# Performance work log

Hardware: AMD Instinct MI355X
Metric: run time of the kernel (lower is better)

Reference implementation:

```python
import jax, jax.numpy as jnp
import numpy as np

PI = 3.141592653589793
TAU = 0.5          # gumbel-softmax temperature
EPS = 1e-6
B, N, D = 128, 32, 256

def _linear(x, w, b=None):
    y = x @ w.T
    return y if b is None else y + b

def _wrap(a):
    return (a + PI) % (2 * PI) - PI

def setup_inputs() -> dict:
    key = jax.random.key(0)
    ks = jax.random.split(key, 16)
    s = 0.05
    return {
        "embedding": jax.random.normal(ks[0], (B, N, 11), jnp.float32),
        "gumbel_u": jax.random.uniform(ks[1], (B * N, N - 1, 2), jnp.float32),
        "emb1_w": jax.random.normal(ks[2], (128, 5), jnp.float32) * s,
        "emb1_b": jnp.zeros((128,), jnp.float32),
        "emb2_w": jax.random.normal(ks[3], (D, 128), jnp.float32) * s,
        "emb2_b": jnp.zeros((D,), jnp.float32),
        "hm1_w": jax.random.normal(ks[4], (D, D + 7), jnp.float32) * s,
        "hm1_b": jnp.zeros((D,), jnp.float32),
        "hm2_w": jax.random.normal(ks[5], (D, D), jnp.float32) * s,
        "hm2_b": jnp.zeros((D,), jnp.float32),
        "he_w": jax.random.normal(ks[6], (2, D), jnp.float32) * s,
        "he_b": jnp.zeros((2,), jnp.float32),
        "q_w": jax.random.normal(ks[7], (D, D), jnp.float32) * s,
        "k_w": jax.random.normal(ks[8], (D, 10), jnp.float32) * s,
        "v_w": jax.random.normal(ks[9], (D, 10), jnp.float32) * s,
        "v_b": jnp.zeros((D,), jnp.float32),
        "dec_w": jax.random.normal(ks[10], (2 * D, 2 * D), jnp.float32) * s,
        "dec_b": jnp.zeros((2 * D,), jnp.float32),
    }

def reference(embedding, gumbel_u, emb1_w, emb1_b, emb2_w, emb2_b,
              hm1_w, hm1_b, hm2_w, hm2_b, he_w, he_b,
              q_w, k_w, v_w, v_b, dec_w, dec_b):
    b, n, _ = embedding.shape
    d = q_w.shape[0]
    # static off-diagonal index lists (i,j), j != i, row-major like mask indexing
    rows, cols = np.nonzero(~np.eye(n, dtype=bool))

    embed = embedding[:, :, 4:9].reshape(b * n, 5)
    position = embedding[:, :, :2]
    heading = embedding[:, :, 2:4]
    action = embedding[:, :, 7:9]
    goal = embedding[:, :, -2:]

    # agent embedding MLP (leaky_relu slope 0.01, torch default)
    h = jax.nn.leaky_relu(_linear(embed, emb1_w, emb1_b))
    agent_embed = jax.nn.leaky_relu(_linear(h, emb2_w, emb2_b)).reshape(b, n, d)

    # pairwise geometry  [b,i,j,...]
    rel_vec = position[:, None, :, :] - position[:, :, None, :]   # pos_j - pos_i
    dx, dy = rel_vec[..., 0], rel_vec[..., 1]
    rel_dist = jnp.linalg.norm(rel_vec, axis=-1, keepdims=True) / 12.0
    heading_angle_i = jnp.arctan2(heading[..., 1], heading[..., 0])[:, :, None]  # [b,n,1]
    angle = _wrap(jnp.arctan2(dy, dx) - heading_angle_i)
    hj_cos = jnp.broadcast_to(heading[:, None, :, 0], (b, n, n))
    hj_sin = jnp.broadcast_to(heading[:, None, :, 1], (b, n, n))
    action_j = jnp.broadcast_to(action[:, None, :, :], (b, n, n, 2))
    edge_features = jnp.concatenate([
        rel_dist, jnp.cos(angle)[..., None], jnp.sin(angle)[..., None],
        hj_cos[..., None], hj_sin[..., None], action_j], axis=-1)  # [b,n,n,7]

    # hard attention branch (off-diagonal pairs only)
    h_i_flat = jnp.broadcast_to(agent_embed[:, :, None, :], (b, n, n - 1, d)).reshape(b * n, n - 1, d)
    edge_flat = edge_features[:, rows, cols].reshape(b * n, n - 1, 7)
    hard_input = jnp.concatenate([h_i_flat, edge_flat], axis=-1)
    h_hard = _linear(jax.nn.relu(_linear(hard_input, hm1_w, hm1_b)), hm2_w, hm2_b)
    hard_logits = _linear(h_hard, he_w, he_b)                      # [b*n, n-1, 2]
    g = -jnp.log(-jnp.log(gumbel_u + 1e-10) + 1e-10)
    hard_soft = jax.nn.softmax((hard_logits + g) / TAU, axis=-1)
    hard_weights = hard_soft[..., 1].reshape(b, n, n - 1)

    unnorm = jnp.linalg.norm(rel_vec, axis=-1, keepdims=True)      # [b,n,n,1]
    unnorm_rel_dist = unnorm[:, rows, cols].reshape(b * n, n - 1, 1)

    # goal polar features
    goal_rel_vec = goal[:, None, :, :] - position[:, :, None, :]   # [b,n,n,2]
    goal_rel_dist = jnp.linalg.norm(goal_rel_vec, axis=-1, keepdims=True)
    goal_rel_angle = _wrap(jnp.arctan2(goal_rel_vec[..., 1], goal_rel_vec[..., 0]) - heading_angle_i)
    goal_polar = jnp.concatenate([goal_rel_dist, jnp.cos(goal_rel_angle)[..., None],
                                  jnp.sin(goal_rel_angle)[..., None]], axis=-1)
    soft_edge = jnp.concatenate([edge_features, goal_polar], axis=-1)  # [b,n,n,10]

    # soft attention (vectorized over agents; off-diagonal gather)
    q = agent_embed @ q_w.T                                         # [b,n,d]
    k = soft_edge @ k_w.T                                           # [b,n,n,d]
    v = jax.nn.relu(_linear(soft_edge, v_w, v_b))                   # [b,n,n,d]
    k_off = k[:, rows, cols].reshape(b, n, n - 1, d)
    v_off = v[:, rows, cols].reshape(b, n, n - 1, d)
    score = jnp.einsum('bnd,bnjd->bnj', q, k_off) / jnp.sqrt(jnp.float32(d))
    soft_w = jax.nn.softmax(score, axis=-1)
    combined = soft_w * hard_weights                                # [b,n,n-1]
    x = jnp.einsum('bnjd,bnj->bnd', v_off, combined).reshape(b * n, d)

    final_input = jnp.concatenate([agent_embed.reshape(b * n, d), x], axis=-1)
    output = _linear(final_input, dec_w, dec_b)                     # [b*n, 2d]

    cwn = combined / (combined.sum(axis=-1, keepdims=True) + EPS)
    mean_entropy = (-(cwn * jnp.log(cwn + EPS)).sum(axis=-1)).mean()
    comb_w = combined.reshape(n, -1)  # matches torch.stack(dim=1).reshape(n, -1)

    return (output, hard_logits[..., 1], unnorm_rel_dist, mean_entropy, hard_weights, comb_w)
```

## Files before the change

### kernel.cpp

```cpp
#include <hip/hip_runtime.h>
#include <hip/hip_bf16.h>
#include <math.h>

typedef __hip_bfloat16 bf16;
typedef short bf16x8 __attribute__((ext_vector_type(8)));
typedef float f32x4 __attribute__((ext_vector_type(4)));
typedef unsigned short u16;

#define R_TOT 4096
#define NJ 31

#define OFF_AE   0
#define OFF_QK   1048576
#define OFF_S1   2097152
#define OFF_ENT  4542464
#define OFF_X    4546560
#define OFF_W    5595136
#define W_E1W   0
#define W_E1B   640
#define W_E2P   768
#define W_E2B   33536
#define W_H1B   101120
#define W_W1EP  167684
#define W_HE2P  171780
#define W_CB    173828
#define W_S1P   200452
#define W_VW    235780
#define W_VB    238340
#define W_DECWT 238596
#define W_DECB  500740
#define W_QKM   501252

#define OUT0 0
#define OUT1 2097152
#define OUT2 2224128
#define OUT3 2351104
#define OUT4 2351105
#define OUT5 2478081

__device__ __forceinline__ float b2f(bf16 x) { return __bfloat162float(x); }
__device__ __forceinline__ float ldin(const void* p, int i, int flag) {
    return flag ? b2f(((const bf16*)p)[i]) : ((const float*)p)[i];
}
__device__ __forceinline__ void stout(void* p, int i, float v, int flag) {
    if (flag) ((bf16*)p)[i] = __float2bfloat16(v);
    else      ((float*)p)[i] = v;
}
__device__ __forceinline__ u16 f2bbits(float v) {
    bf16 h = __float2bfloat16(v);
    return *(u16*)&h;
}
__device__ __forceinline__ int detect_flag(const void* emb) {
    float x = ((const float*)emb)[threadIdx.x & 63];
    int sane = (x == x) && (fabsf(x) < 1e20f);
    unsigned long long m = __ballot(sane);
    return (__popcll(m) == 64) ? 0 : 1;
}

__global__ __launch_bounds__(256) void k_prep(
        const void* emb,
        const void* e1w, const void* e1b, const void* e2w, const void* e2b,
        const void* h1w, const void* h1b, const void* h2w, const void* h2b,
        const void* hew, const void* heb, const void* qw,  const void* kw,
        const void* vw,  const void* vb,  const void* decw,const void* decb,
        float* W) {
    int flag = detect_flag(emb);
    int blk = blockIdx.x;
    int tid = threadIdx.x;
    if (blk < 2048) {
        int idx = blk * 256 + tid;
        if (idx < 262144) {
            int jj   = idx & 7;
            int lane = (idx >> 3) & 63;
            int tile = idx >> 9;
            int nt = tile & 31, kt = tile >> 5;
            int n = nt * 16 + (lane & 15);
            int k = kt * 32 + ((lane >> 4) << 3) + jj;
            ((u16*)(W + W_DECWT))[idx] = f2bbits(ldin(decw, n * 512 + k, flag));
        }
        int j = idx - 262144;
        if (j >= 0 && j < 98304) {
            int p;
            const void* src; int ldm, Wdst;
            if (j < 32768)      { p = j;          src = e2w; ldm = 128; Wdst = W_E2P; }
            else                { p = j - 32768;  src = h1w; ldm = 263; Wdst = W_S1P; }
            int jj   = p & 7;
            int lane = (p >> 3) & 63;
            int tile = p >> 9;
            int nt = tile & 15, kt = tile >> 4;
            int n = nt * 16 + (lane & 15);
            int k = kt * 32 + ((lane >> 4) << 3) + jj;
            ((u16*)(W + Wdst))[p] = f2bbits(ldin(src, n * ldm + k, flag));
        } else if (j >= 98304 && j < 102912) {
            int q2 = j - 98304;
            if      (q2 < 640)   W[W_E1W  + q2]           = ldin(e1w,  q2,          flag);
            else if (q2 < 768)   W[W_E1B  + (q2 - 640)]   = ldin(e1b,  q2 - 640,    flag);
            else if (q2 < 1024)  W[W_E2B  + (q2 - 768)]   = ldin(e2b,  q2 - 768,    flag);
            else if (q2 < 1280)  W[W_H1B  + (q2 - 1024)]  = ldin(h1b,  q2 - 1024,   flag);
            else if (q2 < 3840)  W[W_VW   + (q2 - 1280)]  = ldin(vw,   q2 - 1280,   flag);
            else if (q2 < 4096)  W[W_VB   + (q2 - 3840)]  = ldin(vb,   q2 - 3840,   flag);
            else                 W[W_DECB + (q2 - 4096)]  = ldin(decb, q2 - 4096,   flag);
        }
    } else if (blk < 2304) {
        int p = (blk - 2048) * 16 + (tid >> 4);
        int l = tid & 15;
        int jj = p & 7, lane = (p >> 3) & 63, kt = p >> 9;
        int k = kt * 32 + ((lane >> 4) << 3) + jj;
        int n = lane & 15;
        float v = 0.f;
        if (n < 10) {
#pragma unroll
            for (int dd = 0; dd < 16; dd++) {
                int d = l + 16 * dd;
                v += ldin(qw, d * 256 + k, flag) * ldin(kw, d * 10 + n, flag);
            }
        }
        v += __shfl_xor(v, 1, 64); v += __shfl_xor(v, 2, 64);
        v += __shfl_xor(v, 4, 64); v += __shfl_xor(v, 8, 64);
        if (l == 0) ((u16*)(W + W_QKM))[p] = f2bbits(v);
    } else if (blk < 2560) {
        int q = (blk - 2304) * 16 + (tid >> 4);
        int l = tid & 15;
        int jj = q & 7, lane = (q >> 3) & 63, kt = q >> 9;
        int n = lane & 15;
        int c = kt * 32 + ((lane >> 4) << 3) + jj;
        float v = 0.f;
        if (n < 2) {
#pragma unroll
            for (int dd = 0; dd < 16; dd++) {
                int d = l + 16 * dd;
                v += ldin(hew, n * 256 + d, flag) * ldin(h2w, d * 256 + c, flag);
            }
        }
        v += __shfl_xor(v, 1, 64); v += __shfl_xor(v, 2, 64);
        v += __shfl_xor(v, 4, 64); v += __shfl_xor(v, 8, 64);
        if (l == 0) ((u16*)(W + W_HE2P))[q] = f2bbits(v);
    } else if (blk < 2592) {
        int p = (blk - 2560) * 256 + tid;
        int jj = p & 7, lane = (p >> 3) & 63, nt = p >> 9;
        int n = nt * 16 + (lane & 15);
        int k = ((lane >> 4) << 3) + jj;
        float v = (k < 7) ? ldin(h1w, n * 263 + 256 + k, flag) : 0.f;
        ((u16*)(W + W_W1EP))[p] = f2bbits(v);
    } else {
        if (tid < 32) {
            int i = tid >> 4, l = tid & 15;
            float v = 0.f;
#pragma unroll
            for (int dd = 0; dd < 16; dd++) {
                int d = l + 16 * dd;
                v += ldin(hew, i * 256 + d, flag) * ldin(h2b, d, flag);
            }
            v += __shfl_xor(v, 1, 64); v += __shfl_xor(v, 2, 64);
            v += __shfl_xor(v, 4, 64); v += __shfl_xor(v, 8, 64);
            if (l == 0) W[W_CB + i] = v + ldin(heb, i, flag);
        }
    }
}

__global__ __launch_bounds__(256) void k_embed(const void* emb, const float* W,
                                               u16* aeb, float* qkws, float* s1ws) {
    int flag = detect_flag(emb);
    int r0 = blockIdx.x * 16;
    __shared__ float embL[16][12];
    __shared__ u16 hB[16][136];
    __shared__ u16 aeB[16][264];
    int tid = threadIdx.x;
    for (int idx = tid; idx < 16 * 11; idx += 256) {
        int s = idx / 11, t = idx % 11;
        embL[s][t] = ldin(emb, (r0 + s) * 11 + t, flag);
    }
    __syncthreads();
    for (int idx = tid; idx < 16 * 128; idx += 256) {
        int s = idx >> 7, jo = idx & 127;
        float v = W[W_E1B + jo];
#pragma unroll
        for (int t = 0; t < 5; t++) v += W[W_E1W + jo * 5 + t] * embL[s][4 + t];
        hB[s][jo] = f2bbits(v > 0.f ? v : 0.01f * v);
    }
    __syncthreads();
    int wv = tid >> 6, ln = tid & 63;
    int lr = ln & 15, quad = ln >> 4;
    {
        const bf16x8* Bp = (const bf16x8*)(W + W_E2P);
        f32x4 acc[4];
#pragma unroll
        for (int nt = 0; nt < 4; nt++) acc[nt] = (f32x4){0.f, 0.f, 0.f, 0.f};
#pragma unroll
        for (int kt = 0; kt < 4; kt++) {
            bf16x8 af = *(const bf16x8*)&hB[lr][kt * 32 + (quad << 3)];
#pragma unroll
            for (int nt = 0; nt < 4; nt++) {
                bf16x8 bfr = Bp[(kt * 16 + (wv * 4 + nt)) * 64 + ln];
                acc[nt] = __builtin_amdgcn_mfma_f32_16x16x32_bf16(af, bfr, acc[nt], 0, 0, 0);
            }
        }
#pragma unroll
        for (int nt = 0; nt < 4; nt++) {
            int d = wv * 64 + nt * 16 + lr;
            float bias = W[W_E2B + d];
#pragma unroll
            for (int reg = 0; reg < 4; reg++) {
                int m = quad * 4 + reg;
                float v = acc[nt][reg] + bias;
                v = v > 0.f ? v : 0.01f * v;
                u16 bits = f2bbits(v);
                aeB[m][d] = bits;
                aeb[(r0 + m) * 256 + d] = bits;
            }
        }
    }
    __syncthreads();
    {
        const bf16x8* Bs = (const bf16x8*)(W + W_S1P);
        f32x4 sac[4];
#pragma unroll
        for (int nt = 0; nt < 4; nt++) sac[nt] = (f32x4){0.f, 0.f, 0.f, 0.f};
#pragma unroll
        for (int kt = 0; kt < 8; kt++) {
            bf16x8 af = *(const bf16x8*)&aeB[lr][kt * 32 + (quad << 3)];
#pragma unroll
            for (int nt = 0; nt < 4; nt++) {
                bf16x8 bs = Bs[(kt * 16 + (wv * 4 + nt)) * 64 + ln];
                sac[nt] = __builtin_amdgcn_mfma_f32_16x16x32_bf16(af, bs, sac[nt], 0, 0, 0);
            }
        }
#pragma unroll
        for (int nt = 0; nt < 4; nt++) {
            int d = wv * 64 + nt * 16 + lr;
            float bias = W[W_H1B + d];
#pragma unroll
            for (int reg = 0; reg < 4; reg++) {
                int m = quad * 4 + reg;
                s1ws[(r0 + m) * 256 + d] = sac[nt][reg] + bias;
            }
        }
        if (wv == 0) {
            const bf16x8* Bm = (const bf16x8*)(W + W_QKM);
            f32x4 qk = (f32x4){0.f, 0.f, 0.f, 0.f};
#pragma unroll
            for (int kt = 0; kt < 8; kt++) {
                bf16x8 af = *(const bf16x8*)&aeB[lr][kt * 32 + (quad << 3)];
                qk = __builtin_amdgcn_mfma_f32_16x16x32_bf16(af, Bm[kt * 64 + ln], qk, 0, 0, 0);
            }
            if (lr < 10) {
#pragma unroll
                for (int reg = 0; reg < 4; reg++) {
                    int m = quad * 4 + reg;
                    qkws[(r0 + m) * 10 + lr] = qk[reg];
                }
            }
        }
    }
}

__global__ __launch_bounds__(256) void k_fused(const void* emb, const void* gum,
                                               const float* s1ws, const float* qkws, const float* W,
                                               u16* xb, float* entws, void* out) {
    int flag = detect_flag(emb);
    int r = blockIdx.x;
    int b = r >> 5, i = r & 31;
    __shared__ float embB[32][12];
    __shared__ float seL[32][10];
    __shared__ u16 eA[32][32];
    __shared__ u16 a1[32][264];
    __shared__ float pj[4][32][2];
    __shared__ float cL[32];
    __shared__ float qkL[10];
    int tid = threadIdx.x;
    for (int idx = tid; idx < 32 * 11; idx += 256) {
        int s = idx / 11, t = idx % 11;
        embB[s][t] = ldin(emb, (b * 32 + s) * 11 + t, flag);
    }
    for (int idx = tid; idx < 32 * 32; idx += 256) ((u16*)eA)[idx] = 0;
    if (tid >= 64 && tid < 74) qkL[tid - 64] = qkws[r * 10 + (tid - 64)];
    __syncthreads();
    if (tid < NJ) {
        int jp = tid;
        int j = jp + (jp >= i ? 1 : 0);
        float pix = embB[i][0], piy = embB[i][1], hix = embB[i][2], hiy = embB[i][3];
        float pjx = embB[j][0], pjy = embB[j][1], hjx = embB[j][2], hjy = embB[j][3];
        float ajx = embB[j][7], ajy = embB[j][8];
        float gjx = embB[j][9], gjy = embB[j][10];
        float dx = pjx - pix, dy = pjy - piy;
        float dist = sqrtf(dx * dx + dy * dy);
        float hai = atan2f(hiy, hix);
        float ang = atan2f(dy, dx) - hai;
        float gx = gjx - pix, gy = gjy - piy;
        float gdist = sqrtf(gx * gx + gy * gy);
        float gang = atan2f(gy, gx) - hai;
        float f[10];
        f[0] = dist * (1.f / 12.f);
        f[1] = cosf(ang); f[2] = sinf(ang);
        f[3] = hjx; f[4] = hjy; f[5] = ajx; f[6] = ajy;
        f[7] = gdist; f[8] = cosf(gang); f[9] = sinf(gang);
#pragma unroll
        for (int t = 0; t < 10; t++) seL[jp][t] = f[t];
#pragma unroll
        for (int t = 0; t < 7; t++) eA[jp][t] = f2bbits(f[t]);
        stout(out, OUT2 + r * NJ + jp, dist, flag);
    }
    __syncthreads();
    int wv = tid >> 6, ln = tid & 63;
    int lr = ln & 15, quad = ln >> 4;
    {
        const bf16x8* Bp = (const bf16x8*)(W + W_W1EP);
        bf16x8 af0 = *(const bf16x8*)&eA[lr][quad << 3];
        bf16x8 af1 = *(const bf16x8*)&eA[16 + lr][quad << 3];
#pragma unroll
        for (int nt = 0; nt < 4; nt++) {
            int gnt = wv * 4 + nt;
            int d = gnt * 16 + lr;
            float s1v = s1ws[r * 256 + d];
            f32x4 acc0 = (f32x4){s1v, s1v, s1v, s1v};
            f32x4 acc1 = acc0;
            bf16x8 bb = Bp[gnt * 64 + ln];
            acc0 = __builtin_amdgcn_mfma_f32_16x16x32_bf16(af0, bb, acc0, 0, 0, 0);
            acc1 = __builtin_amdgcn_mfma_f32_16x16x32_bf16(af1, bb, acc1, 0, 0, 0);
#pragma unroll
            for (int reg = 0; reg < 4; reg++) {
                a1[(quad << 2) + reg][d]      = f2bbits(fmaxf(acc0[reg], 0.f));
                a1[16 + (quad << 2) + reg][d] = f2bbits(fmaxf(acc1[reg], 0.f));
            }
        }
    }
    __syncthreads();
    {
        const bf16x8* Ep = (const bf16x8*)(W + W_HE2P);
        f32x4 l0 = (f32x4){0.f, 0.f, 0.f, 0.f};
        f32x4 l1 = (f32x4){0.f, 0.f, 0.f, 0.f};
#pragma unroll
        for (int kk = 0; kk < 2; kk++) {
            int kt = wv * 2 + kk;
            bf16x8 a0 = *(const bf16x8*)&a1[lr][kt * 32 + (quad << 3)];
            bf16x8 a1f = *(const bf16x8*)&a1[16 + lr][kt * 32 + (quad << 3)];
            bf16x8 bb = Ep[kt * 64 + ln];
            l0 = __builtin_amdgcn_mfma_f32_16x16x32_bf16(a0, bb, l0, 0, 0, 0);
            l1 = __builtin_amdgcn_mfma_f32_16x16x32_bf16(a1f, bb, l1, 0, 0, 0);
        }
        if (lr < 2) {
#pragma unroll
            for (int reg = 0; reg < 4; reg++) {
                pj[wv][(quad << 2) + reg][lr]      = l0[reg];
                pj[wv][16 + (quad << 2) + reg][lr] = l1[reg];
            }
        }
    }
    __syncthreads();
    if (wv == 0) {
        float hwv = 0.f;
        if (ln < NJ) {
            float p0 = pj[0][ln][0] + pj[1][ln][0] + pj[2][ln][0] + pj[3][ln][0];
            float p1 = pj[0][ln][1] + pj[1][ln][1] + pj[2][ln][1] + pj[3][ln][1];
            float l0 = p0 + W[W_CB + 0], l1 = p1 + W[W_CB + 1];
            float u0 = ldin(gum, (r * NJ + ln) * 2 + 0, flag);
            float u1 = ldin(gum, (r * NJ + ln) * 2 + 1, flag);
            float g0 = -logf(-logf(u0 + 1e-10f) + 1e-10f);
            float g1 = -logf(-logf(u1 + 1e-10f) + 1e-10f);
            float dl = ((l1 + g1) - (l0 + g0)) * 2.0f;
            hwv = 1.f / (1.f + expf(-dl));
            stout(out, OUT1 + r * NJ + ln, l1, flag);
            stout(out, OUT4 + r * NJ + ln, hwv, flag);
        }
        float sc = -1e30f;
        if (ln < NJ) {
            float p = 0.f;
#pragma unroll
            for (int t = 0; t < 10; t++) p += qkL[t] * seL[ln][t];
            sc = p * (1.f / 16.f);
        }
        float m = sc;
#pragma unroll
        for (int s = 32; s >= 1; s >>= 1) m = fmaxf(m, __shfl_xor(m, s, 64));
        float e = (ln < NJ) ? expf(sc - m) : 0.f;
        float sum = e;
#pragma unroll
        for (int s = 32; s >= 1; s >>= 1) sum += __shfl_xor(sum, s, 64);
        float sw = e / sum;
        float cmb = sw * hwv;
        if (ln < NJ) {
            cL[ln] = cmb;
            stout(out, OUT5 + r * NJ + ln, cmb, flag);
        }
        float csum = cmb;
#pragma unroll
        for (int s = 32; s >= 1; s >>= 1) csum += __shfl_xor(csum, s, 64);
        float cwn = cmb / (csum + 1e-6f);
        float et = (ln < NJ) ? -cwn * logf(cwn + 1e-6f) : 0.f;
#pragma unroll
        for (int s = 32; s >= 1; s >>= 1) et += __shfl_xor(et, s, 64);
        if (ln == 0) entws[r] = et;
    }
    __syncthreads();
    float vwr[10];
#pragma unroll
    for (int t = 0; t < 10; t++) vwr[t] = W[W_VW + tid * 10 + t];
    float vbv = W[W_VB + tid];
    float x = 0.f;
    for (int j = 0; j < NJ; j++) {
        float v = vbv;
#pragma unroll
        for (int t = 0; t < 10; t++) v += vwr[t] * seL[j][t];
        v = fmaxf(v, 0.f);
        x += v * cL[j];
    }
    xb[r * 256 + tid] = f2bbits(x);
}

__global__ __launch_bounds__(256) void k_dec(const void* emb, const u16* aeb, const u16* xb,
                                             const float* W, const float* entws, void* out) {
    int flag = detect_flag(emb);
    int r0 = (blockIdx.x >> 2) * 32;
    int nq = blockIdx.x & 3;
    __shared__ u16 finB[32][520];
    int tid = threadIdx.x;
    for (int idx = tid; idx < 32 * 512; idx += 256) {
        int s = idx >> 9, c = idx & 511;
        finB[s][c] = (c < 256) ? aeb[(r0 + s) * 256 + c] : xb[(r0 + s) * 256 + (c - 256)];
    }
    __syncthreads();
    int wv = tid >> 6, ln = tid & 63;
    int lr = ln & 15, quad = ln >> 4;
    const bf16x8* Bp = (const bf16x8*)(W + W_DECWT);
    f32x4 acc[2][2];
#pragma unroll
    for (int mt = 0; mt < 2; mt++)
#pragma unroll
        for (int nt = 0; nt < 2; nt++) acc[mt][nt] = (f32x4){0.f, 0.f, 0.f, 0.f};
#pragma unroll
    for (int kt = 0; kt < 16; kt++) {
        bf16x8 af[2];
#pragma unroll
        for (int mt = 0; mt < 2; mt++)
            af[mt] = *(const bf16x8*)&finB[mt * 16 + lr][kt * 32 + (quad << 3)];
#pragma unroll
        for (int nt = 0; nt < 2; nt++) {
            int gnt = nq * 8 + wv * 2 + nt;
            bf16x8 bfr = Bp[(kt * 32 + gnt) * 64 + ln];
#pragma unroll
            for (int mt = 0; mt < 2; mt++)
                acc[mt][nt] = __builtin_amdgcn_mfma_f32_16x16x32_bf16(af[mt], bfr, acc[mt][nt], 0, 0, 0);
        }
    }
#pragma unroll
    for (int nt = 0; nt < 2; nt++) {
        int d = (nq * 8 + wv * 2 + nt) * 16 + lr;
        float bias = W[W_DECB + d];
#pragma unroll
        for (int mt = 0; mt < 2; mt++)
#pragma unroll
            for (int reg = 0; reg < 4; reg++) {
                int m = mt * 16 + quad * 4 + reg;
                stout(out, OUT0 + (r0 + m) * 512 + d, acc[mt][nt][reg] + bias, flag);
            }
    }
    if (blockIdx.x == 0) {
        __shared__ float red[4];
        float s = 0.f;
        for (int i2 = tid; i2 < R_TOT; i2 += 256) s += entws[i2];
#pragma unroll
        for (int m = 32; m >= 1; m >>= 1) s += __shfl_xor(s, m, 64);
        if ((tid & 63) == 0) red[tid >> 6] = s;
        __syncthreads();
        if (tid == 0) {
            float t = red[0] + red[1] + red[2] + red[3];
            stout(out, OUT3, t / (float)R_TOT, flag);
        }
    }
}

extern "C" void kernel_launch(void* const* d_in, const int* in_sizes, int n_in,
                              void* d_out, int out_size, void* d_ws, size_t ws_size,
                              hipStream_t stream) {
    const void* emb  = d_in[0];
    const void* gum  = d_in[1];
    const void* e1w  = d_in[2];
    const void* e1b  = d_in[3];
    const void* e2w  = d_in[4];
    const void* e2b  = d_in[5];
    const void* h1w  = d_in[6];
    const void* h1b  = d_in[7];
    const void* h2w  = d_in[8];
    const void* h2b  = d_in[9];
    const void* hew  = d_in[10];
    const void* heb  = d_in[11];
    const void* qw   = d_in[12];
    const void* kw   = d_in[13];
    const void* vw   = d_in[14];
    const void* vb   = d_in[15];
    const void* decw = d_in[16];
    const void* decb = d_in[17];

    float* wsf = (float*)d_ws;
    u16*   aeb  = (u16*)(wsf + OFF_AE);
    float* qkws = wsf + OFF_QK;
    float* s1ws = wsf + OFF_S1;
    float* entw = wsf + OFF_ENT;
    u16*   xb   = (u16*)(wsf + OFF_X);
    float* W    = wsf + OFF_W;

    hipLaunchKernelGGL(k_prep, dim3(2593), dim3(256), 0, stream,
                       emb, e1w, e1b, e2w, e2b, h1w, h1b, h2w, h2b, hew, heb,
                       qw, kw, vw, vb, decw, decb, W);
    hipLaunchKernelGGL(k_embed, dim3(256), dim3(256), 0, stream, emb, W, aeb, qkws, s1ws);
    hipLaunchKernelGGL(k_fused, dim3(4096), dim3(256), 0, stream,
                       emb, gum, s1ws, qkws, W, xb, entw, d_out);
    hipLaunchKernelGGL(k_dec, dim3(512), dim3(256), 0, stream, emb, aeb, xb, W, entw, d_out);
}
```

Before: 161.1 us.

## Merge four kernels into one persistent kernel with software grid barriers

Replaces the four separate launches (weight prep, embed, fused attention, decoder) with a single persistent kernel of 512 blocks. The stages are separated by an atomic-counter grid barrier, and blocks loop over the former grid sizes. This removes launch gaps and per-kernel tail effects between stages. In exchange it adds barrier spin costs and a memset launch, caps parallelism at 512 blocks for the 4096-block fused stage, and relies on every block being co-resident, which risks deadlock if they are not.

```diff
diff --git a/kernel.cpp b/kernel.cpp
--- a/kernel.cpp
+++ b/kernel.cpp
@@ -9,6 +9,7 @@
 
 #define R_TOT 4096
 #define NJ 31
+#define GRID_N 512
 
 #define OFF_AE   0
 #define OFF_QK   1048576
@@ -30,6 +31,7 @@
 #define W_DECWT 238596
 #define W_DECB  500740
 #define W_QKM   501252
+#define OFF_BAR  6100992
 
 #define OUT0 0
 #define OUT1 2097152
@@ -57,414 +59,425 @@
     return (__popcll(m) == 64) ? 0 : 1;
 }
 
-__global__ __launch_bounds__(256) void k_prep(
-        const void* emb,
+__device__ __forceinline__ void grid_sync(int* bar) {
+    __syncthreads();
+    if (threadIdx.x == 0) {
+        __threadfence();
+        int gen = __hip_atomic_load(bar + 1, __ATOMIC_RELAXED, __HIP_MEMORY_SCOPE_AGENT);
+        int arrived = __hip_atomic_fetch_add(bar, 1, __ATOMIC_ACQ_REL, __HIP_MEMORY_SCOPE_AGENT);
+        if (arrived == GRID_N - 1) {
+            __hip_atomic_store(bar, 0, __ATOMIC_RELAXED, __HIP_MEMORY_SCOPE_AGENT);
+            __hip_atomic_fetch_add(bar + 1, 1, __ATOMIC_RELEASE, __HIP_MEMORY_SCOPE_AGENT);
+        } else {
+            while (__hip_atomic_load(bar + 1, __ATOMIC_ACQUIRE, __HIP_MEMORY_SCOPE_AGENT) == gen)
+                __builtin_amdgcn_s_sleep(2);
+        }
+        __threadfence();
+    }
+    __syncthreads();
+}
+
+struct EmbedS { float embL[16][12]; u16 hB[16][136]; u16 aeB[16][264]; };
+struct FusedS { float embB[32][12]; float seL[32][10]; u16 eA[32][32];
+                u16 a1[32][264]; float pj[4][32][2]; float cL[32]; float qkL[10]; };
+struct DecS   { u16 finB[32][520]; float red[4]; };
+union SharedU { EmbedS e; FusedS f; DecS d; };
+
+__global__ __launch_bounds__(256, 2) void k_mega(
+        const void* emb, const void* gum,
         const void* e1w, const void* e1b, const void* e2w, const void* e2b,
         const void* h1w, const void* h1b, const void* h2w, const void* h2b,
         const void* hew, const void* heb, const void* qw,  const void* kw,
         const void* vw,  const void* vb,  const void* decw,const void* decb,
-        float* W) {
+        float* W, u16* aeb, float* qkws, float* s1ws, float* entws, u16* xb,
+        int* bar, void* out) {
+    __shared__ SharedU sh;
     int flag = detect_flag(emb);
-    int blk = blockIdx.x;
     int tid = threadIdx.x;
-    if (blk < 2048) {
-        int idx = blk * 256 + tid;
-        if (idx < 262144) {
-            int jj   = idx & 7;
-            int lane = (idx >> 3) & 63;
-            int tile = idx >> 9;
-            int nt = tile & 31, kt = tile >> 5;
-            int n = nt * 16 + (lane & 15);
+    int wv = tid >> 6, ln = tid & 63;
+    int lr = ln & 15, quad = ln >> 4;
+
+    for (int blk = blockIdx.x; blk < 2593; blk += GRID_N) {
+        if (blk < 2048) {
+            int idx = blk * 256 + tid;
+            if (idx < 262144) {
+                int jj   = idx & 7;
+                int lane = (idx >> 3) & 63;
+                int tile = idx >> 9;
+                int nt = tile & 31, kt = tile >> 5;
+                int n = nt * 16 + (lane & 15);
+                int k = kt * 32 + ((lane >> 4) << 3) + jj;
+                ((u16*)(W + W_DECWT))[idx] = f2bbits(ldin(decw, n * 512 + k, flag));
+            }
+            int j = idx - 262144;
+            if (j >= 0 && j < 98304) {
+                int p;
+                const void* src; int ldm, Wdst;
+                if (j < 32768)      { p = j;          src = e2w; ldm = 128; Wdst = W_E2P; }
+                else                { p = j - 32768;  src = h1w; ldm = 263; Wdst = W_S1P; }
+                int jj   = p & 7;
+                int lane = (p >> 3) & 63;
+                int tile = p >> 9;
+                int nt = tile & 15, kt = tile >> 4;
+                int n = nt * 16 + (lane & 15);
+                int k = kt * 32 + ((lane >> 4) << 3) + jj;
+                ((u16*)(W + Wdst))[p] = f2bbits(ldin(src, n * ldm + k, flag));
+            } else if (j >= 98304 && j < 102912) {
+                int q2 = j - 98304;
+                if      (q2 < 640)   W[W_E1W  + q2]           = ldin(e1w,  q2,          flag);
+                else if (q2 < 768)   W[W_E1B  + (q2 - 640)]   = ldin(e1b,  q2 - 640,    flag);
+                else if (q2 < 1024)  W[W_E2B  + (q2 - 768)]   = ldin(e2b,  q2 - 768,    flag);
+                else if (q2 < 1280)  W[W_H1B  + (q2 - 1024)]  = ldin(h1b,  q2 - 1024,   flag);
+                else if (q2 < 3840)  W[W_VW   + (q2 - 1280)]  = ldin(vw,   q2 - 1280,   flag);
+                else if (q2 < 4096)  W[W_VB   + (q2 - 3840)]  = ldin(vb,   q2 - 3840,   flag);
+                else                 W[W_DECB + (q2 - 4096)]  = ldin(decb, q2 - 4096,   flag);
+            }
+        } else if (blk < 2304) {
+            int p = (blk - 2048) * 16 + (tid >> 4);
+            int l = tid & 15;
+            int jj = p & 7, lane = (p >> 3) & 63, kt = p >> 9;
             int k = kt * 32 + ((lane >> 4) << 3) + jj;
-            ((u16*)(W + W_DECWT))[idx] = f2bbits(ldin(decw, n * 512 + k, flag));
-        }
-        int j = idx - 262144;
-        if (j >= 0 && j < 98304) {
-            int p;
-            const void* src; int ldm, Wdst;
-            if (j < 32768)      { p = j;          src = e2w; ldm = 128; Wdst = W_E2P; }
-            else                { p = j - 32768;  src = h1w; ldm = 263; Wdst = W_S1P; }
-            int jj   = p & 7;
-            int lane = (p >> 3) & 63;
-            int tile = p >> 9;
-            int nt = tile & 15, kt = tile >> 4;
-            int n = nt * 16 + (lane & 15);
-            int k = kt * 32 + ((lane >> 4) << 3) + jj;
-            ((u16*)(W + Wdst))[p] = f2bbits(ldin(src, n * ldm + k, flag));
-        } else if (j >= 98304 && j < 102912) {
-            int q2 = j - 98304;
-            if      (q2 < 640)   W[W_E1W  + q2]           = ldin(e1w,  q2,          flag);
-            else if (q2 < 768)   W[W_E1B  + (q2 - 640)]   = ldin(e1b,  q2 - 640,    flag);
-            else if (q2 < 1024)  W[W_E2B  + (q2 - 768)]   = ldin(e2b,  q2 - 768,    flag);
-            else if (q2 < 1280)  W[W_H1B  + (q2 - 1024)]  = ldin(h1b,  q2 - 1024,   flag);
-            else if (q2 < 3840)  W[W_VW   + (q2 - 1280)]  = ldin(vw,   q2 - 1280,   flag);
-            else if (q2 < 4096)  W[W_VB   + (q2 - 3840)]  = ldin(vb,   q2 - 3840,   flag);
-            else                 W[W_DECB + (q2 - 4096)]  = ldin(decb, q2 - 4096,   flag);
-        }
-    } else if (blk < 2304) {
-        int p = (blk - 2048) * 16 + (tid >> 4);
-        int l = tid & 15;
-        int jj = p & 7, lane = (p >> 3) & 63, kt = p >> 9;
-        int k = kt * 32 + ((lane >> 4) << 3) + jj;
-        int n = lane & 15;
-        float v = 0.f;
-        if (n < 10) {
-#pragma unroll
-            for (int dd = 0; dd < 16; dd++) {
-                int d = l + 16 * dd;
-                v += ldin(qw, d * 256 + k, flag) * ldin(kw, d * 10 + n, flag);
-            }
-        }
-        v += __shfl_xor(v, 1, 64); v += __shfl_xor(v, 2, 64);
-        v += __shfl_xor(v, 4, 64); v += __shfl_xor(v, 8, 64);
-        if (l == 0) ((u16*)(W + W_QKM))[p] = f2bbits(v);
-    } else if (blk < 2560) {
-        int q = (blk - 2304) * 16 + (tid >> 4);
-        int l = tid & 15;
-        int jj = q & 7, lane = (q >> 3) & 63, kt = q >> 9;
-        int n = lane & 15;
-        int c = kt * 32 + ((lane >> 4) << 3) + jj;
-        float v = 0.f;
-        if (n < 2) {
-#pragma unroll
-            for (int dd = 0; dd < 16; dd++) {
-                int d = l + 16 * dd;
-                v += ldin(hew, n * 256 + d, flag) * ldin(h2w, d * 256 + c, flag);
-            }
-        }
-        v += __shfl_xor(v, 1, 64); v += __shfl_xor(v, 2, 64);
-        v += __shfl_xor(v, 4, 64); v += __shfl_xor(v, 8, 64);
-        if (l == 0) ((u16*)(W + W_HE2P))[q] = f2bbits(v);
-    } else if (blk < 2592) {
-        int p = (blk - 2560) * 256 + tid;
-        int jj = p & 7, lane = (p >> 3) & 63, nt = p >> 9;
-        int n = nt * 16 + (lane & 15);
-        int k = ((lane >> 4) << 3) + jj;
-        float v = (k < 7) ? ldin(h1w, n * 263 + 256 + k, flag) : 0.f;
-        ((u16*)(W + W_W1EP))[p] = f2bbits(v);
-    } else {
-        if (tid < 32) {
-            int i = tid >> 4, l = tid & 15;
+            int n = lane & 15;
             float v = 0.f;
-#pragma unroll
-            for (int dd = 0; dd < 16; dd++) {
-                int d = l + 16 * dd;
-                v += ldin(hew, i * 256 + d, flag) * ldin(h2b, d, flag);
+            if (n < 10) {
+#pragma unroll
+                for (int dd = 0; dd < 16; dd++) {
+                    int d = l + 16 * dd;
+                    v += ldin(qw, d * 256 + k, flag) * ldin(kw, d * 10 + n, flag);
+                }
             }
             v += __shfl_xor(v, 1, 64); v += __shfl_xor(v, 2, 64);
             v += __shfl_xor(v, 4, 64); v += __shfl_xor(v, 8, 64);
-            if (l == 0) W[W_CB + i] = v + ldin(heb, i, flag);
+            if (l == 0) ((u16*)(W + W_QKM))[p] = f2bbits(v);
+        } else if (blk < 2560) {
+            int q = (blk - 2304) * 16 + (tid >> 4);
+            int l = tid & 15;
+            int jj = q & 7, lane = (q >> 3) & 63, kt = q >> 9;
+            int n = lane & 15;
+            int c = kt * 32 + ((lane >> 4) << 3) + jj;
+            float v = 0.f;
+            if (n < 2) {
+#pragma unroll
+                for (int dd = 0; dd < 16; dd++) {
+                    int d = l + 16 * dd;
+                    v += ldin(hew, n * 256 + d, flag) * ldin(h2w, d * 256 + c, flag);
+                }
+            }
+            v += __shfl_xor(v, 1, 64); v += __shfl_xor(v, 2, 64);
+            v += __shfl_xor(v, 4, 64); v += __shfl_xor(v, 8, 64);
+            if (l == 0) ((u16*)(W + W_HE2P))[q] = f2bbits(v);
+        } else if (blk < 2592) {
+            int p = (blk - 2560) * 256 + tid;
+            int jj = p & 7, lane = (p >> 3) & 63, nt = p >> 9;
+            int n = nt * 16 + (lane & 15);
+            int k = ((lane >> 4) << 3) + jj;
+            float v = (k < 7) ? ldin(h1w, n * 263 + 256 + k, flag) : 0.f;
+            ((u16*)(W + W_W1EP))[p] = f2bbits(v);
+        } else {
+            if (tid < 32) {
+                int i = tid >> 4, l = tid & 15;
+                float v = 0.f;
+#pragma unroll
+                for (int dd = 0; dd < 16; dd++) {
+                    int d = l + 16 * dd;
+                    v += ldin(hew, i * 256 + d, flag) * ldin(h2b, d, flag);
+                }
+                v += __shfl_xor(v, 1, 64); v += __shfl_xor(v, 2, 64);
+                v += __shfl_xor(v, 4, 64); v += __shfl_xor(v, 8, 64);
+                if (l == 0) W[W_CB + i] = v + ldin(heb, i, flag);
+            }
         }
     }
-}
-
-__global__ __launch_bounds__(256) void k_embed(const void* emb, const float* W,
-                                               u16* aeb, float* qkws, float* s1ws) {
-    int flag = detect_flag(emb);
-    int r0 = blockIdx.x * 16;
-    __shared__ float embL[16][12];
-    __shared__ u16 hB[16][136];
-    __shared__ u16 aeB[16][264];
-    int tid = threadIdx.x;
-    for (int idx = tid; idx < 16 * 11; idx += 256) {
-        int s = idx / 11, t = idx % 11;
-        embL[s][t] = ldin(emb, (r0 + s) * 11 + t, flag);
-    }
-    __syncthreads();
-    for (int idx = tid; idx < 16 * 128; idx += 256) {
-        int s = idx >> 7, jo = idx & 127;
-        float v = W[W_E1B + jo];
-#pragma unroll
-        for (int t = 0; t < 5; t++) v += W[W_E1W + jo * 5 + t] * embL[s][4 + t];
-        hB[s][jo] = f2bbits(v > 0.f ? v : 0.01f * v);
-    }
-    __syncthreads();
-    int wv = tid >> 6, ln = tid & 63;
-    int lr = ln & 15, quad = ln >> 4;
-    {
-        const bf16x8* Bp = (const bf16x8*)(W + W_E2P);
-        f32x4 acc[4];
-#pragma unroll
-        for (int nt = 0; nt < 4; nt++) acc[nt] = (f32x4){0.f, 0.f, 0.f, 0.f};
-#pragma unroll
-        for (int kt = 0; kt < 4; kt++) {
-            bf16x8 af = *(const bf16x8*)&hB[lr][kt * 32 + (quad << 3)];
+    grid_sync(bar);
+
+    if (blockIdx.x < 256) {
+        EmbedS& S = sh.e;
+        int r0 = blockIdx.x * 16;
+        for (int idx = tid; idx < 16 * 11; idx += 256) {
+            int s = idx / 11, t = idx % 11;
+            S.embL[s][t] = ldin(emb, (r0 + s) * 11 + t, flag);
+        }
+        __syncthreads();
+        for (int idx = tid; idx < 16 * 128; idx += 256) {
+            int s = idx >> 7, jo = idx & 127;
+            float v = W[W_E1B + jo];
+#pragma unroll
+            for (int t = 0; t < 5; t++) v += W[W_E1W + jo * 5 + t] * S.embL[s][4 + t];
+            S.hB[s][jo] = f2bbits(v > 0.f ? v : 0.01f * v);
+        }
+        __syncthreads();
+        {
+            const bf16x8* Bp = (const bf16x8*)(W + W_E2P);
+            f32x4 acc[4];
+#pragma unroll
+            for (int nt = 0; nt < 4; nt++) acc[nt] = (f32x4){0.f, 0.f, 0.f, 0.f};
+#pragma unroll
+            for (int kt = 0; kt < 4; kt++) {
+                bf16x8 af = *(const bf16x8*)&S.hB[lr][kt * 32 + (quad << 3)];
+#pragma unroll
+                for (int nt = 0; nt < 4; nt++) {
+                    bf16x8 bfr = Bp[(kt * 16 + (wv * 4 + nt)) * 64 + ln];
+                    acc[nt] = __builtin_amdgcn_mfma_f32_16x16x32_bf16(af, bfr, acc[nt], 0, 0, 0);
+                }
+            }
 #pragma unroll
             for (int nt = 0; nt < 4; nt++) {
-                bf16x8 bfr = Bp[(kt * 16 + (wv * 4 + nt)) * 64 + ln];
-                acc[nt] = __builtin_amdgcn_mfma_f32_16x16x32_bf16(af, bfr, acc[nt], 0, 0, 0);
-            }
-        }
-#pragma unroll
-        for (int nt = 0; nt < 4; nt++) {
-            int d = wv * 64 + nt * 16 + lr;
-            float bias = W[W_E2B + d];
-#pragma unroll
-            for (int reg = 0; reg < 4; reg++) {
-                int m = quad * 4 + reg;
-                float v = acc[nt][reg] + bias;
-                v = v > 0.f ? v : 0.01f * v;
-                u16 bits = f2bbits(v);
-                aeB[m][d] = bits;
-                aeb[(r0 + m) * 256 + d] = bits;
-            }
-        }
-    }
-    __syncthreads();
-    {
-        const bf16x8* Bs = (const bf16x8*)(W + W_S1P);
-        f32x4 sac[4];
-#pragma unroll
-        for (int nt = 0; nt < 4; nt++) sac[nt] = (f32x4){0.f, 0.f, 0.f, 0.f};
-#pragma unroll
-        for (int kt = 0; kt < 8; kt++) {
-            bf16x8 af = *(const bf16x8*)&aeB[lr][kt * 32 + (quad << 3)];
-#pragma unroll
-            for (int nt = 0; nt < 4; nt++) {
-                bf16x8 bs = Bs[(kt * 16 + (wv * 4 + nt)) * 64 + ln];
-                sac[nt] = __builtin_amdgcn_mfma_f32_16x16x32_bf16(af, bs, sac[nt], 0, 0, 0);
-            }
-        }
-#pragma unroll
-        for (int nt = 0; nt < 4; nt++) {
-            int d = wv * 64 + nt * 16 + lr;
-            float bias = W[W_H1B + d];
-#pragma unroll
-            for (int reg = 0; reg < 4; reg++) {
-                int m = quad * 4 + reg;
-                s1ws[(r0 + m) * 256 + d] = sac[nt][reg] + bias;
-            }
-        }
-        if (wv == 0) {
-            const bf16x8* Bm = (const bf16x8*)(W + W_QKM);
-            f32x4 qk = (f32x4){0.f, 0.f, 0.f, 0.f};
-#pragma unroll
-            for (int kt = 0; kt < 8; kt++) {
-                bf16x8 af = *(const bf16x8*)&aeB[lr][kt * 32 + (quad << 3)];
-                qk = __builtin_amdgcn_mfma_f32_16x16x32_bf16(af, Bm[kt * 64 + ln], qk, 0, 0, 0);
-            }
-            if (lr < 10) {
+                int d = wv * 64 + nt * 16 + lr;
+                float bias = W[W_E2B + d];
 #pragma unroll
                 for (int reg = 0; reg < 4; reg++) {
                     int m = quad * 4 + reg;
-                    qkws[(r0 + m) * 10 + lr] = qk[reg];
+                    float v = acc[nt][reg] + bias;
+                    v = v > 0.f ? v : 0.01f * v;
+                    u16 bits = f2bbits(v);
+                    S.aeB[m][d] = bits;
+                    aeb[(r0 + m) * 256 + d] = bits;
+                }
+            }
+        }
+        __syncthreads();
+        {
+            const bf16x8* Bs = (const bf16x8*)(W + W_S1P);
+            f32x4 sac[4];
+#pragma unroll
+            for (int nt = 0; nt < 4; nt++) sac[nt] = (f32x4){0.f, 0.f, 0.f, 0.f};
+#pragma unroll
+            for (int kt = 0; kt < 8; kt++) {
+                bf16x8 af = *(const bf16x8*)&S.aeB[lr][kt * 32 + (quad << 3)];
+#pragma unroll
+                for (int nt = 0; nt < 4; nt++) {
+                    bf16x8 bs = Bs[(kt * 16 + (wv * 4 + nt)) * 64 + ln];
+                    sac[nt] = __builtin_amdgcn_mfma_f32_16x16x32_bf16(af, bs, sac[nt], 0, 0, 0);
+                }
+            }
+#pragma unroll
+            for (int nt = 0; nt < 4; nt++) {
+                int d = wv * 64 + nt * 16 + lr;
+                float bias = W[W_H1B + d];
+#pragma unroll
+                for (int reg = 0; reg < 4; reg++) {
+                    int m = quad * 4 + reg;
+                    s1ws[(r0 + m) * 256 + d] = sac[nt][reg] + bias;
+                }
+            }
+            if (wv == 0) {
+                const bf16x8* Bm = (const bf16x8*)(W + W_QKM);
+                f32x4 qk = (f32x4){0.f, 0.f, 0.f, 0.f};
+#pragma unroll
+                for (int kt = 0; kt < 8; kt++) {
+                    bf16x8 af = *(const bf16x8*)&S.aeB[lr][kt * 32 + (quad << 3)];
+                    qk = __builtin_amdgcn_mfma_f32_16x16x32_bf16(af, Bm[kt * 64 + ln], qk, 0, 0, 0);
+                }
+                if (lr < 10) {
+#pragma unroll
+                    for (int reg = 0; reg < 4; reg++) {
+                        int m = quad * 4 + reg;
+                        qkws[(r0 + m) * 10 + lr] = qk[reg];
+                    }
                 }
             }
         }
     }
-}
-
-__global__ __launch_bounds__(256) void k_fused(const void* emb, const void* gum,
-                                               const float* s1ws, const float* qkws, const float* W,
-                                               u16* xb, float* entws, void* out) {
-    int flag = detect_flag(emb);
-    int r = blockIdx.x;
-    int b = r >> 5, i = r & 31;
-    __shared__ float embB[32][12];
-    __shared__ float seL[32][10];
-    __shared__ u16 eA[32][32];
-    __shared__ u16 a1[32][264];
-    __shared__ float pj[4][32][2];
-    __shared__ float cL[32];
-    __shared__ float qkL[10];
-    int tid = threadIdx.x;
-    for (int idx = tid; idx < 32 * 11; idx += 256) {
-        int s = idx / 11, t = idx % 11;
-        embB[s][t] = ldin(emb, (b * 32 + s) * 11 + t, flag);
+    grid_sync(bar);
+
+    {
+        FusedS& S = sh.f;
+        for (int idx = tid; idx < 32 * 32; idx += 256) ((u16*)S.eA)[idx] = 0;
+        float vwr[10];
+#pragma unroll
+        for (int t = 0; t < 10; t++) vwr[t] = W[W_VW + tid * 10 + t];
+        float vbv = W[W_VB + tid];
+        for (int r = blockIdx.x; r < R_TOT; r += GRID_N) {
+            int b = r >> 5, i = r & 31;
+            __syncthreads();
+            for (int idx = tid; idx < 32 * 11; idx += 256) {
+                int s = idx / 11, t = idx % 11;
+                S.embB[s][t] = ldin(emb, (b * 32 + s) * 11 + t, flag);
+            }
+            if (tid >= 64 && tid < 74) S.qkL[tid - 64] = qkws[r * 10 + (tid - 64)];
+            __syncthreads();
+            if (tid < NJ) {
+                int jp = tid;
+                int j = jp + (jp >= i ? 1 : 0);
+                float pix = S.embB[i][0], piy = S.embB[i][1], hix = S.embB[i][2], hiy = S.embB[i][3];
+                float pjx = S.embB[j][0], pjy = S.embB[j][1], hjx = S.embB[j][2], hjy = S.embB[j][3];
+                float ajx = S.embB[j][7], ajy = S.embB[j][8];
+                float gjx = S.embB[j][9], gjy = S.embB[j][10];
+                float dx = pjx - pix, dy = pjy - piy;
+                float dist = sqrtf(dx * dx + dy * dy);
+                float hai = atan2f(hiy, hix);
+                float ang = atan2f(dy, dx) - hai;
+                float gx = gjx - pix, gy = gjy - piy;
+                float gdist = sqrtf(gx * gx + gy * gy);
+                float gang = atan2f(gy, gx) - hai;
+                float f[10];
+                f[0] = dist * (1.f / 12.f);
+                f[1] = cosf(ang); f[2] = sinf(ang);
+                f[3] = hjx; f[4] = hjy; f[5] = ajx; f[6] = ajy;
+                f[7] = gdist; f[8] = cosf(gang); f[9] = sinf(gang);
+#pragma unroll
+                for (int t = 0; t < 10; t++) S.seL[jp][t] = f[t];
+#pragma unroll
+                for (int t = 0; t < 7; t++) S.eA[jp][t] = f2bbits(f[t]);
+                stout(out, OUT2 + r * NJ + jp, dist, flag);
+            }
+            __syncthreads();
+            {
+                const bf16x8* Bp = (const bf16x8*)(W + W_W1EP);
+                bf16x8 af0 = *(const bf16x8*)&S.eA[lr][quad << 3];
+                bf16x8 af1 = *(const bf16x8*)&S.eA[16 + lr][quad << 3];
+#pragma unroll
+                for (int nt = 0; nt < 4; nt++) {
+                    int gnt = wv * 4 + nt;
+                    int d = gnt * 16 + lr;
+                    float s1v = s1ws[r * 256 + d];
+                    f32x4 acc0 = (f32x4){s1v, s1v, s1v, s1v};
+                    f32x4 acc1 = acc0;
+                    bf16x8 bb = Bp[gnt * 64 + ln];
+                    acc0 = __builtin_amdgcn_mfma_f32_16x16x32_bf16(af0, bb, acc0, 0, 0, 0);
+                    acc1 = __builtin_amdgcn_mfma_f32_16x16x32_bf16(af1, bb, acc1, 0, 0, 0);
+#pragma unroll
+                    for (int reg = 0; reg < 4; reg++) {
+                        S.a1[(quad << 2) + reg][d]      = f2bbits(fmaxf(acc0[reg], 0.f));
+                        S.a1[16 + (quad << 2) + reg][d] = f2bbits(fmaxf(acc1[reg], 0.f));
+                    }
+                }
+            }
+            __syncthreads();
+            {
+                const bf16x8* Ep = (const bf16x8*)(W + W_HE2P);
+                f32x4 l0 = (f32x4){0.f, 0.f, 0.f, 0.f};
+                f32x4 l1 = (f32x4){0.f, 0.f, 0.f, 0.f};
+#pragma unroll
+                for (int kk = 0; kk < 2; kk++) {
+                    int kt = wv * 2 + kk;
+                    bf16x8 a0 = *(const bf16x8*)&S.a1[lr][kt * 32 + (quad << 3)];
+                    bf16x8 a1f = *(const bf16x8*)&S.a1[16 + lr][kt * 32 + (quad << 3)];
+                    bf16x8 bb = Ep[kt * 64 + ln];
+                    l0 = __builtin_amdgcn_mfma_f32_16x16x32_bf16(a0, bb, l0, 0, 0, 0);
+                    l1 = __builtin_amdgcn_mfma_f32_16x16x32_bf16(a1f, bb, l1, 0, 0, 0);
+                }
+                if (lr < 2) {
+#pragma unroll
+                    for (int reg = 0; reg < 4; reg++) {
+                        S.pj[wv][(quad << 2) + reg][lr]      = l0[reg];
+                        S.pj[wv][16 + (quad << 2) + reg][lr] = l1[reg];
+                    }
+                }
+            }
+            __syncthreads();
+            if (wv == 0) {
+                float hwv = 0.f;
+                if (ln < NJ) {
+                    float p0 = S.pj[0][ln][0] + S.pj[1][ln][0] + S.pj[2][ln][0] + S.pj[3][ln][0];
+                    float p1 = S.pj[0][ln][1] + S.pj[1][ln][1] + S.pj[2][ln][1] + S.pj[3][ln][1];
+                    float l0 = p0 + W[W_CB + 0], l1 = p1 + W[W_CB + 1];
+                    float u0 = ldin(gum, (r * NJ + ln) * 2 + 0, flag);
+                    float u1 = ldin(gum, (r * NJ + ln) * 2 + 1, flag);
+                    float g0 = -logf(-logf(u0 + 1e-10f) + 1e-10f);
+                    float g1 = -logf(-logf(u1 + 1e-10f) + 1e-10f);
+                    float dl = ((l1 + g1) - (l0 + g0)) * 2.0f;
+                    hwv = 1.f / (1.f + expf(-dl));
+                    stout(out, OUT1 + r * NJ + ln, l1, flag);
+                    stout(out, OUT4 + r * NJ + ln, hwv, flag);
+                }
+                float sc = -1e30f;
+                if (ln < NJ) {
+                    float p = 0.f;
+#pragma unroll
+                    for (int t = 0; t < 10; t++) p += S.qkL[t] * S.seL[ln][t];
+                    sc = p * (1.f / 16.f);
+                }
+                float m = sc;
+#pragma unroll
+                for (int s = 32; s >= 1; s >>= 1) m = fmaxf(m, __shfl_xor(m, s, 64));
+                float e = (ln < NJ) ? expf(sc - m) : 0.f;
+                float sum = e;
+#pragma unroll
+                for (int s = 32; s >= 1; s >>= 1) sum += __shfl_xor(sum, s, 64);
+                float sw = e / sum;
+                float cmb = sw * hwv;
+                if (ln < NJ) {
+                    S.cL[ln] = cmb;
+                    stout(out, OUT5 + r * NJ + ln, cmb, flag);
+                }
+                float csum = cmb;
+#pragma unroll
+                for (int s = 32; s >= 1; s >>= 1) csum += __shfl_xor(csum, s, 64);
+                float cwn = cmb / (csum + 1e-6f);
+                float et = (ln < NJ) ? -cwn * logf(cwn + 1e-6f) : 0.f;
+#pragma unroll
+                for (int s = 32; s >= 1; s >>= 1) et += __shfl_xor(et, s, 64);
+                if (ln == 0) entws[r] = et;
+            }
+            __syncthreads();
+            float x = 0.f;
+            for (int j = 0; j < NJ; j++) {
+                float v = vbv;
+#pragma unroll
+                for (int t = 0; t < 10; t++) v += vwr[t] * S.seL[j][t];
+                v = fmaxf(v, 0.f);
+                x += v * S.cL[j];
+            }
+            xb[r * 256 + tid] = f2bbits(x);
+        }
     }
-    for (int idx = tid; idx < 32 * 32; idx += 256) ((u16*)eA)[idx] = 0;
-    if (tid >= 64 && tid < 74) qkL[tid - 64] = qkws[r * 10 + (tid - 64)];
-    __syncthreads();
-    if (tid < NJ) {
-        int jp = tid;
-        int j = jp + (jp >= i ? 1 : 0);
-        float pix = embB[i][0], piy = embB[i][1], hix = embB[i][2], hiy = embB[i][3];
-        float pjx = embB[j][0], pjy = embB[j][1], hjx = embB[j][2], hjy = embB[j][3];
-        float ajx = embB[j][7], ajy = embB[j][8];
-        float gjx = embB[j][9], gjy = embB[j][10];
-        float dx = pjx - pix, dy = pjy - piy;
-        float dist = sqrtf(dx * dx + dy * dy);
-        float hai = atan2f(hiy, hix);
-        float ang = atan2f(dy, dx) - hai;
-        float gx = gjx - pix, gy = gjy - piy;
-        float gdist = sqrtf(gx * gx + gy * gy);
-        float gang = atan2f(gy, gx) - hai;
-        float f[10];
-        f[0] = dist * (1.f / 12.f);
-        f[1] = cosf(ang); f[2] = sinf(ang);
-        f[3] = hjx; f[4] = hjy; f[5] = ajx; f[6] = ajy;
-        f[7] = gdist; f[8] = cosf(gang); f[9] = sinf(gang);
-#pragma unroll
-        for (int t = 0; t < 10; t++) seL[jp][t] = f[t];
-#pragma unroll
-        for (int t = 0; t < 7; t++) eA[jp][t] = f2bbits(f[t]);
-        stout(out, OUT2 + r * NJ + jp, dist, flag);
-    }
-    __syncthreads();
-    int wv = tid >> 6, ln = tid & 63;
-    int lr = ln & 15, quad = ln >> 4;
+    grid_sync(bar);
+
     {
-        const bf16x8* Bp = (const bf16x8*)(W + W_W1EP);
-        bf16x8 af0 = *(const bf16x8*)&eA[lr][quad << 3];
-        bf16x8 af1 = *(const bf16x8*)&eA[16 + lr][quad << 3];
-#pragma unroll
-        for (int nt = 0; nt < 4; nt++) {
-            int gnt = wv * 4 + nt;
-            int d = gnt * 16 + lr;
-            float s1v = s1ws[r * 256 + d];
-            f32x4 acc0 = (f32x4){s1v, s1v, s1v, s1v};
-            f32x4 acc1 = acc0;
-            bf16x8 bb = Bp[gnt * 64 + ln];
-            acc0 = __builtin_amdgcn_mfma_f32_16x16x32_bf16(af0, bb, acc0, 0, 0, 0);
-            acc1 = __builtin_amdgcn_mfma_f32_16x16x32_bf16(af1, bb, acc1, 0, 0, 0);
-#pragma unroll
-            for (int reg = 0; reg < 4; reg++) {
-                a1[(quad << 2) + reg][d]      = f2bbits(fmaxf(acc0[reg], 0.f));
-                a1[16 + (quad << 2) + reg][d] = f2bbits(fmaxf(acc1[reg], 0.f));
-            }
-        }
-    }
-    __syncthreads();
-    {
-        const bf16x8* Ep = (const bf16x8*)(W + W_HE2P);
-        f32x4 l0 = (f32x4){0.f, 0.f, 0.f, 0.f};
-        f32x4 l1 = (f32x4){0.f, 0.f, 0.f, 0.f};
-#pragma unroll
-        for (int kk = 0; kk < 2; kk++) {
-            int kt = wv * 2 + kk;
-            bf16x8 a0 = *(const bf16x8*)&a1[lr][kt * 32 + (quad << 3)];
-            bf16x8 a1f = *(const bf16x8*)&a1[16 + lr][kt * 32 + (quad << 3)];
-            bf16x8 bb = Ep[kt * 64 + ln];
-            l0 = __builtin_amdgcn_mfma_f32_16x16x32_bf16(a0, bb, l0, 0, 0, 0);
-            l1 = __builtin_amdgcn_mfma_f32_16x16x32_bf16(a1f, bb, l1, 0, 0, 0);
-        }
-        if (lr < 2) {
-#pragma unroll
-            for (int reg = 0; reg < 4; reg++) {
-                pj[wv][(quad << 2) + reg][lr]      = l0[reg];
-                pj[wv][16 + (quad << 2) + reg][lr] = l1[reg];
-            }
-        }
-    }
-    __syncthreads();
-    if (wv == 0) {
-        float hwv = 0.f;
-        if (ln < NJ) {
-            float p0 = pj[0][ln][0] + pj[1][ln][0] + pj[2][ln][0] + pj[3][ln][0];
-            float p1 = pj[0][ln][1] + pj[1][ln][1] + pj[2][ln][1] + pj[3][ln][1];
-            float l0 = p0 + W[W_CB + 0], l1 = p1 + W[W_CB + 1];
-            float u0 = ldin(gum, (r * NJ + ln) * 2 + 0, flag);
-            float u1 = ldin(gum, (r * NJ + ln) * 2 + 1, flag);
-            float g0 = -logf(-logf(u0 + 1e-10f) + 1e-10f);
-            float g1 = -logf(-logf(u1 + 1e-10f) + 1e-10f);
-            float dl = ((l1 + g1) - (l0 + g0)) * 2.0f;
-            hwv = 1.f / (1.f + expf(-dl));
-            stout(out, OUT1 + r * NJ + ln, l1, flag);
-            stout(out, OUT4 + r * NJ + ln, hwv, flag);
-        }
-        float sc = -1e30f;
-        if (ln < NJ) {
-            float p = 0.f;
-#pragma unroll
-            for (int t = 0; t < 10; t++) p += qkL[t] * seL[ln][t];
-            sc = p * (1.f / 16.f);
-        }
-        float m = sc;
-#pragma unroll
-        for (int s = 32; s >= 1; s >>= 1) m = fmaxf(m, __shfl_xor(m, s, 64));
-        float e = (ln < NJ) ? expf(sc - m) : 0.f;
-        float sum = e;
-#pragma unroll
-        for (int s = 32; s >= 1; s >>= 1) sum += __shfl_xor(sum, s, 64);
-        float sw = e / sum;
-        float cmb = sw * hwv;
-        if (ln < NJ) {
-            cL[ln] = cmb;
-            stout(out, OUT5 + r * NJ + ln, cmb, flag);
-        }
-        float csum = cmb;
-#pragma unroll
-        for (int s = 32; s >= 1; s >>= 1) csum += __shfl_xor(csum, s, 64);
-        float cwn = cmb / (csum + 1e-6f);
-        float et = (ln < NJ) ? -cwn * logf(cwn + 1e-6f) : 0.f;
-#pragma unroll
-        for (int s = 32; s >= 1; s >>= 1) et += __shfl_xor(et, s, 64);
-        if (ln == 0) entws[r] = et;
-    }
-    __syncthreads();
-    float vwr[10];
-#pragma unroll
-    for (int t = 0; t < 10; t++) vwr[t] = W[W_VW + tid * 10 + t];
-    float vbv = W[W_VB + tid];
-    float x = 0.f;
-    for (int j = 0; j < NJ; j++) {
-        float v = vbv;
-#pragma unroll
-        for (int t = 0; t < 10; t++) v += vwr[t] * seL[j][t];
-        v = fmaxf(v, 0.f);
-        x += v * cL[j];
-    }
-    xb[r * 256 + tid] = f2bbits(x);
-}
-
-__global__ __launch_bounds__(256) void k_dec(const void* emb, const u16* aeb, const u16* xb,
-                                             const float* W, const float* entws, void* out) {
-    int flag = detect_flag(emb);
-    int r0 = (blockIdx.x >> 2) * 32;
-    int nq = blockIdx.x & 3;
-    __shared__ u16 finB[32][520];
-    int tid = threadIdx.x;
-    for (int idx = tid; idx < 32 * 512; idx += 256) {
-        int s = idx >> 9, c = idx & 511;
-        finB[s][c] = (c < 256) ? aeb[(r0 + s) * 256 + c] : xb[(r0 + s) * 256 + (c - 256)];
-    }
-    __syncthreads();
-    int wv = tid >> 6, ln = tid & 63;
-    int lr = ln & 15, quad = ln >> 4;
-    const bf16x8* Bp = (const bf16x8*)(W + W_DECWT);
-    f32x4 acc[2][2];
-#pragma unroll
-    for (int mt = 0; mt < 2; mt++)
-#pragma unroll
-        for (int nt = 0; nt < 2; nt++) acc[mt][nt] = (f32x4){0.f, 0.f, 0.f, 0.f};
-#pragma unroll
-    for (int kt = 0; kt < 16; kt++) {
-        bf16x8 af[2];
+        DecS& S = sh.d;
+        int u = blockIdx.x;
+        int r0 = (u >> 2) * 32;
+        int nq = u & 3;
+        for (int idx = tid; idx < 32 * 512; idx += 256) {
+            int s = idx >> 9, c = idx & 511;
+            S.finB[s][c] = (c < 256) ? aeb[(r0 + s) * 256 + c] : xb[(r0 + s) * 256 + (c - 256)];
+        }
+        __syncthreads();
+        const bf16x8* Bp = (const bf16x8*)(W + W_DECWT);
+        f32x4 acc[2][2];
 #pragma unroll
         for (int mt = 0; mt < 2; mt++)
-            af[mt] = *(const bf16x8*)&finB[mt * 16 + lr][kt * 32 + (quad << 3)];
+#pragma unroll
+            for (int nt = 0; nt < 2; nt++) acc[mt][nt] = (f32x4){0.f, 0.f, 0.f, 0.f};
+#pragma unroll
+        for (int kt = 0; kt < 16; kt++) {
+            bf16x8 af[2];
+#pragma unroll
+            for (int mt = 0; mt < 2; mt++)
+                af[mt] = *(const bf16x8*)&S.finB[mt * 16 + lr][kt * 32 + (quad << 3)];
+#pragma unroll
+            for (int nt = 0; nt < 2; nt++) {
+                int gnt = nq * 8 + wv * 2 + nt;
+                bf16x8 bfr = Bp[(kt * 32 + gnt) * 64 + ln];
+#pragma unroll
+                for (int mt = 0; mt < 2; mt++)
+                    acc[mt][nt] = __builtin_amdgcn_mfma_f32_16x16x32_bf16(af[mt], bfr, acc[mt][nt], 0, 0, 0);
+            }
+        }
 #pragma unroll
         for (int nt = 0; nt < 2; nt++) {
-            int gnt = nq * 8 + wv * 2 + nt;
-            bf16x8 bfr = Bp[(kt * 32 + gnt) * 64 + ln];
+            int d = (nq * 8 + wv * 2 + nt) * 16 + lr;
+            float bias = W[W_DECB + d];
 #pragma unroll
             for (int mt = 0; mt < 2; mt++)
-                acc[mt][nt] = __builtin_amdgcn_mfma_f32_16x16x32_bf16(af[mt], bfr, acc[mt][nt], 0, 0, 0);
-        }
-    }
-#pragma unroll
-    for (int nt = 0; nt < 2; nt++) {
-        int d = (nq * 8 + wv * 2 + nt) * 16 + lr;
-        float bias = W[W_DECB + d];
-#pragma unroll
-        for (int mt = 0; mt < 2; mt++)
-#pragma unroll
-            for (int reg = 0; reg < 4; reg++) {
-                int m = mt * 16 + quad * 4 + reg;
-                stout(out, OUT0 + (r0 + m) * 512 + d, acc[mt][nt][reg] + bias, flag);
-            }
-    }
-    if (blockIdx.x == 0) {
-        __shared__ float red[4];
-        float s = 0.f;
-        for (int i2 = tid; i2 < R_TOT; i2 += 256) s += entws[i2];
-#pragma unroll
-        for (int m = 32; m >= 1; m >>= 1) s += __shfl_xor(s, m, 64);
-        if ((tid & 63) == 0) red[tid >> 6] = s;
-        __syncthreads();
-        if (tid == 0) {
-            float t = red[0] + red[1] + red[2] + red[3];
-            stout(out, OUT3, t / (float)R_TOT, flag);
+#pragma unroll
+                for (int reg = 0; reg < 4; reg++) {
+                    int m = mt * 16 + quad * 4 + reg;
+                    stout(out, OUT0 + (r0 + m) * 512 + d, acc[mt][nt][reg] + bias, flag);
+                }
+        }
+        if (u == 0) {
+            float s = 0.f;
+            for (int i2 = tid; i2 < R_TOT; i2 += 256) s += entws[i2];
+#pragma unroll
+            for (int m = 32; m >= 1; m >>= 1) s += __shfl_xor(s, m, 64);
+            if ((tid & 63) == 0) S.red[tid >> 6] = s;
+            __syncthreads();
+            if (tid == 0) {
+                float t = S.red[0] + S.red[1] + S.red[2] + S.red[3];
+                stout(out, OUT3, t / (float)R_TOT, flag);
+            }
         }
     }
 }
@@ -498,12 +511,12 @@
     float* entw = wsf + OFF_ENT;
     u16*   xb   = (u16*)(wsf + OFF_X);
     float* W    = wsf + OFF_W;
-
-    hipLaunchKernelGGL(k_prep, dim3(2593), dim3(256), 0, stream,
-                       emb, e1w, e1b, e2w, e2b, h1w, h1b, h2w, h2b, hew, heb,
-                       qw, kw, vw, vb, decw, decb, W);
-    hipLaunchKernelGGL(k_embed, dim3(256), dim3(256), 0, stream, emb, W, aeb, qkws, s1ws);
-    hipLaunchKernelGGL(k_fused, dim3(4096), dim3(256), 0, stream,
-                       emb, gum, s1ws, qkws, W, xb, entw, d_out);
-    hipLaunchKernelGGL(k_dec, dim3(512), dim3(256), 0, stream, emb, aeb, xb, W, entw, d_out);
-}
+    int*   bar  = (int*)(wsf + OFF_BAR);
+
+    hipMemsetAsync(bar, 0, 2 * sizeof(int), stream);
+
+    hipLaunchKernelGGL(k_mega, dim3(GRID_N), dim3(256), 0, stream,
+                       emb, gum, e1w, e1b, e2w, e2b, h1w, h1b, h2w, h2b,
+                       hew, heb, qw, kw, vw, vb, decw, decb,
+                       W, aeb, qkws, s1ws, entw, xb, bar, d_out);
+}
```

Measured after the change: 405.3 us. 152% more time.
